# Optimization experiments

Measured on AMD Instinct MI355X. Metric: run time of the kernel, lower is better.

The kernel has to match this reference:

```python
import jax, jax.numpy as jnp
import numpy as np


def sinusoidal_pe(d, length, dtype=jnp.float32):
    """Standard transformer sin/cos positional encoding along the W axis.
    Returns (d, length): pe[2i, p] = sin(p/10000^(2i/d)), pe[2i+1, p] = cos(...)."""
    pos = jnp.arange(length, dtype=dtype)[None, :]            # (1, W)
    i = jnp.arange(0, d, 2, dtype=dtype)[:, None]             # (d//2, 1)
    div = jnp.exp(-i * (np.log(10000.0) / d))                 # (d//2, 1)
    ang = pos * div                                           # (d//2, W)
    pe = jnp.zeros((d, length), dtype)
    pe = pe.at[0::2].set(jnp.sin(ang)).at[1::2].set(jnp.cos(ang))
    return pe


def setup_inputs() -> dict:
    key = jax.random.key(0)
    ks = jax.random.split(key, 8)
    B, C, D, H, W = 2, 64, 32, 64, 96
    q_k_dim = 32
    s = 1.0 / np.sqrt(C)
    return {
        "x": jax.random.normal(ks[0], (B, C, D, H, W), jnp.float32),
        "Wq": jax.random.normal(ks[1], (q_k_dim, C), jnp.float32) * s,
        "bq": jax.random.normal(ks[2], (q_k_dim,), jnp.float32) * 0.01,
        "Wk": jax.random.normal(ks[3], (q_k_dim, C), jnp.float32) * s,
        "bk": jax.random.normal(ks[4], (q_k_dim,), jnp.float32) * 0.01,
        "Wv": jax.random.normal(ks[5], (C, C), jnp.float32) * s,
        "bv": jax.random.normal(ks[6], (C,), jnp.float32) * 0.01,
        "gamma": jax.random.normal(ks[7], (1,), jnp.float32) * 0.1,
    }


def reference(x, Wq, bq, Wk, bk, Wv, bv, gamma):
    # x: (B, C, D, H, W)
    B, C, D, H, W = x.shape
    qk = Wq.shape[0]
    # 1x1x1 Conv3d == per-voxel channel matmul
    Q = jnp.einsum('bcdhw,qc->bqdhw', x, Wq) + bq[None, :, None, None, None]
    K = jnp.einsum('bcdhw,qc->bqdhw', x, Wk) + bk[None, :, None, None, None]
    V = jnp.einsum('bcdhw,vc->bvdhw', x, Wv) + bv[None, :, None, None, None]
    # additive sinusoidal positional encoding along the row (W) axis
    pe_qk = sinusoidal_pe(qk, W, x.dtype)[None, :, None, None, :]
    pe_v = sinusoidal_pe(C, W, x.dtype)[None, :, None, None, :]
    Q = Q + pe_qk
    K = K + pe_qk
    V = V + pe_v
    # row attention: scores over the W axis, independently per (b, d, h)
    # attn[b,d,h,i,j] = sum_q Q[b,q,d,h,i] * K[b,q,d,h,j]  (no 1/sqrt(d) scaling, as in source)
    attn = jax.nn.softmax(jnp.einsum('bqdhi,bqdhj->bdhij', Q, K), axis=-1)
    # out[b,c,d,h,i] = sum_j V[b,c,d,h,j] * attn[b,d,h,i,j]
    out = jnp.einsum('bcdhj,bdhij->bcdhi', V, attn)
    return gamma * out + x
```

## Files before the change

### kernel.cpp

```cpp
#include <hip/hip_runtime.h>
#include <hip/hip_bf16.h>
#include <math.h>

constexpr int Cc = 64, Dd = 32, Hh = 64, Ww = 96, QKd = 32;
constexpr int CSTRIDE = Dd * Hh * Ww;
constexpr int BDIM = 256;

#define FREQ_QK 0.28782313662425574f
#define FREQ_V  0.14391156831212787f
#define LOG2E   1.44269504088896340736f

typedef __bf16 bf16_t;
typedef bf16_t bf16x8 __attribute__((ext_vector_type(8)));
typedef bf16_t bf16x4 __attribute__((ext_vector_type(4)));
typedef float  floatx4 __attribute__((ext_vector_type(4)));

constexpr int XS_STRIDE = 72;
constexpr int QS_STRIDE = 32;
constexpr int VS_STRIDE = 104;
constexpr int PS_STRIDE = 104;
constexpr int OFF_QS = 6912;
constexpr int OFF_KS = 6912 + 3072;
constexpr int OFF_VS = OFF_KS + 3072;
constexpr int SMEM_ELEMS = OFF_VS + 6656;

__global__ __launch_bounds__(BDIM, 4)
void row_attn_mfma(const float* __restrict__ x,
                   const float* __restrict__ Wq, const float* __restrict__ bq,
                   const float* __restrict__ Wk, const float* __restrict__ bk,
                   const float* __restrict__ Wv, const float* __restrict__ bv,
                   const float* __restrict__ gamma,
                   float* __restrict__ y)
{
    __shared__ __align__(16) bf16_t smem[SMEM_ELEMS];
    bf16_t* Xs = smem;
    bf16_t* Ps = smem;
    bf16_t* Qs = smem + OFF_QS;
    bf16_t* Ks = smem + OFF_KS;
    bf16_t* Vs = smem + OFF_VS;

    const int t    = threadIdx.x;
    const int lane = t & 63;
    const int wid  = t >> 6;
    const int l16  = lane & 15;
    const int quad = lane >> 4;

    const int bid = blockIdx.x;
    const int b   = bid / (Dd * Hh);
    const int rem = bid % (Dd * Hh);
    const int d   = rem / Hh;
    const int h   = rem % Hh;
    const int base0 = b * (Cc * CSTRIDE) + d * (Hh * Ww) + h * Ww;

#pragma unroll
    for (int k = 0; k < 12; ++k) {
        int idx = t + k * BDIM;
        int w  = idx % Ww;
        int c  = (idx / Ww) * 2;
        float v0 = x[base0 + c * CSTRIDE + w];
        float v1 = x[base0 + (c + 1) * CSTRIDE + w];
        unsigned short u0 = __builtin_bit_cast(unsigned short, (bf16_t)v0);
        unsigned short u1 = __builtin_bit_cast(unsigned short, (bf16_t)v1);
        *(unsigned int*)(&Xs[w * XS_STRIDE + c]) = (unsigned)u0 | ((unsigned)u1 << 16);
    }

    const float* Wmat = (wid == 0) ? Wq : (wid == 1) ? Wk : Wv;
    const float* bias = (wid == 0) ? bq : (wid == 1) ? bk : bv;
    const float freqc = (wid < 2) ? FREQ_QK : FREQ_V;
    const int   mbase = (wid == 3) ? 32 : 0;

    bf16x8 wfrag[2][2];
#pragma unroll
    for (int mt = 0; mt < 2; ++mt)
#pragma unroll
        for (int kt = 0; kt < 2; ++kt) {
            const float* p = Wmat + (mbase + mt * 16 + l16) * 64 + kt * 32 + quad * 8;
            float4 lo = *(const float4*)p;
            float4 hi = *(const float4*)(p + 4);
            bf16x8 f;
            f[0] = (bf16_t)lo.x; f[1] = (bf16_t)lo.y; f[2] = (bf16_t)lo.z; f[3] = (bf16_t)lo.w;
            f[4] = (bf16_t)hi.x; f[5] = (bf16_t)hi.y; f[6] = (bf16_t)hi.z; f[7] = (bf16_t)hi.w;
            wfrag[mt][kt] = f;
        }
    float biasv[2][4], freq2[2][2];
#pragma unroll
    for (int mt = 0; mt < 2; ++mt) {
#pragma unroll
        for (int r = 0; r < 4; ++r)
            biasv[mt][r] = bias[mbase + mt * 16 + quad * 4 + r];
#pragma unroll
        for (int p2 = 0; p2 < 2; ++p2)
            freq2[mt][p2] = __expf(-(float)(mbase + mt * 16 + quad * 4 + 2 * p2) * freqc);
    }
    __syncthreads();

    bf16_t* dstQK = (wid == 0) ? Qs : Ks;
#pragma unroll
    for (int nt = 0; nt < 6; ++nt) {
        bf16x8 bfr[2];
#pragma unroll
        for (int kt = 0; kt < 2; ++kt)
            bfr[kt] = *(const bf16x8*)(&Xs[(nt * 16 + l16) * XS_STRIDE + kt * 32 + quad * 8]);
#pragma unroll
        for (int mt = 0; mt < 2; ++mt) {
            floatx4 acc = {0.f, 0.f, 0.f, 0.f};
            acc = __builtin_amdgcn_mfma_f32_16x16x32_bf16(wfrag[mt][0], bfr[0], acc, 0, 0, 0);
            acc = __builtin_amdgcn_mfma_f32_16x16x32_bf16(wfrag[mt][1], bfr[1], acc, 0, 0, 0);
            float wv = (float)(nt * 16 + l16);
            float out[4];
#pragma unroll
            for (int p2 = 0; p2 < 2; ++p2) {
                float sn, cs;
                __sincosf(wv * freq2[mt][p2], &sn, &cs);
                out[2 * p2]     = acc[2 * p2]     + biasv[mt][2 * p2]     + sn;
                out[2 * p2 + 1] = acc[2 * p2 + 1] + biasv[mt][2 * p2 + 1] + cs;
            }
            if (wid < 2) {
                if (wid == 0) {
#pragma unroll
                    for (int r = 0; r < 4; ++r) out[r] *= LOG2E;
                }
                bf16x4 pk;
                pk[0] = (bf16_t)out[0]; pk[1] = (bf16_t)out[1];
                pk[2] = (bf16_t)out[2]; pk[3] = (bf16_t)out[3];
                const int w  = nt * 16 + l16;
                const int el = (w * QS_STRIDE + mt * 16 + quad * 4) ^ ((w & 7) << 3);
                *(bf16x4*)(&dstQK[el]) = pk;
            } else {
#pragma unroll
                for (int r = 0; r < 4; ++r)
                    Vs[(mbase + mt * 16 + quad * 4 + r) * VS_STRIDE + nt * 16 + l16] = (bf16_t)out[r];
            }
        }
    }
    __syncthreads();

    const int it0 = (wid < 2) ? wid * 2 : wid + 2;
    const int itc = (wid < 2) ? 2 : 1;
    bf16x8 qfr[2];
#pragma unroll
    for (int ii = 0; ii < 2; ++ii) {
        const int it = it0 + ((itc == 2) ? ii : 0);
        const int w  = it * 16 + l16;
        qfr[ii] = *(const bf16x8*)(&Qs[(w * QS_STRIDE + quad * 8) ^ ((w & 7) << 3)]);
    }
    bf16x8 kfr[6];
#pragma unroll
    for (int jt = 0; jt < 6; ++jt) {
        const int w = jt * 16 + l16;
        kfr[jt] = *(const bf16x8*)(&Ks[(w * QS_STRIDE + quad * 8) ^ ((w & 7) << 3)]);
    }
    __syncthreads();

    for (int ii = 0; ii < itc; ++ii) {
        const int it = it0 + ii;
        floatx4 sacc[6];
#pragma unroll
        for (int jt = 0; jt < 6; ++jt) {
            floatx4 z = {0.f, 0.f, 0.f, 0.f};
            sacc[jt] = __builtin_amdgcn_mfma_f32_16x16x32_bf16(kfr[jt], qfr[ii], z, 0, 0, 0);
        }
        float mr[6];
#pragma unroll
        for (int jt = 0; jt < 6; ++jt)
            mr[jt] = fmaxf(fmaxf(sacc[jt][0], sacc[jt][1]), fmaxf(sacc[jt][2], sacc[jt][3]));
        float m = fmaxf(fmaxf(fmaxf(mr[0], mr[1]), fmaxf(mr[2], mr[3])), fmaxf(mr[4], mr[5]));
        m = fmaxf(m, __shfl_xor(m, 16));
        m = fmaxf(m, __shfl_xor(m, 32));
        float sum = 0.f;
#pragma unroll
        for (int jt = 0; jt < 6; ++jt) {
#pragma unroll
            for (int r = 0; r < 4; ++r) {
                float e = exp2f(sacc[jt][r] - m);
                sacc[jt][r] = e;
                sum += e;
            }
        }
        sum += __shfl_xor(sum, 16);
        sum += __shfl_xor(sum, 32);
        const float inv = __builtin_amdgcn_rcpf(sum);
        const int row = it * 16 + l16;
#pragma unroll
        for (int jt = 0; jt < 6; ++jt) {
            bf16x4 pk;
            pk[0] = (bf16_t)(sacc[jt][0] * inv);
            pk[1] = (bf16_t)(sacc[jt][1] * inv);
            pk[2] = (bf16_t)(sacc[jt][2] * inv);
            pk[3] = (bf16_t)(sacc[jt][3] * inv);
            *(bf16x4*)(&Ps[row * PS_STRIDE + jt * 16 + quad * 4]) = pk;
        }
    }
    __syncthreads();

    const float g = gamma[0];
    const int ct = wid;
    bf16x8 vfr[3];
#pragma unroll
    for (int ks = 0; ks < 3; ++ks)
        vfr[ks] = *(const bf16x8*)(&Vs[(ct * 16 + l16) * VS_STRIDE + ks * 32 + quad * 8]);
#pragma unroll
    for (int it = 0; it < 6; ++it) {
        floatx4 acc = {0.f, 0.f, 0.f, 0.f};
#pragma unroll
        for (int ks = 0; ks < 3; ++ks) {
            bf16x8 bfr = *(const bf16x8*)(&Ps[(it * 16 + l16) * PS_STRIDE + ks * 32 + quad * 8]);
            acc = __builtin_amdgcn_mfma_f32_16x16x32_bf16(vfr[ks], bfr, acc, 0, 0, 0);
        }
#pragma unroll
        for (int r = 0; r < 4; ++r) {
            int c  = ct * 16 + quad * 4 + r;
            int gi = base0 + c * CSTRIDE + it * 16 + l16;
            y[gi] = fmaf(g, acc[r], x[gi]);
        }
    }
}

extern "C" void kernel_launch(void* const* d_in, const int* in_sizes, int n_in,
                              void* d_out, int out_size, void* d_ws, size_t ws_size,
                              hipStream_t stream) {
    const float* x     = (const float*)d_in[0];
    const float* Wq    = (const float*)d_in[1];
    const float* bq    = (const float*)d_in[2];
    const float* Wk    = (const float*)d_in[3];
    const float* bk    = (const float*)d_in[4];
    const float* Wv    = (const float*)d_in[5];
    const float* bv    = (const float*)d_in[6];
    const float* gamma = (const float*)d_in[7];
    float* y = (float*)d_out;

    dim3 grid(2 * 32 * 64);
    row_attn_mfma<<<grid, BDIM, 0, stream>>>(x, Wq, bq, Wk, bk, Wv, bv, gamma, y);
}
```

Before: 214.2 us.

## Process four rows per block with register prefetch of next row

Each block now handles four consecutive H rows, loading the next row's x values into registers while the current row is computed. Weight fragments, biases and positional-encoding seeds are set up once per block. Per-column sincos is replaced by an angle-addition rotation recurrence. This trades fewer, longer-lived blocks and higher register pressure for amortized setup and overlapped global loads.

```diff
diff --git a/kernel.cpp b/kernel.cpp
--- a/kernel.cpp
+++ b/kernel.cpp
@@ -5,6 +5,7 @@
 constexpr int Cc = 64, Dd = 32, Hh = 64, Ww = 96, QKd = 32;
 constexpr int CSTRIDE = Dd * Hh * Ww;
 constexpr int BDIM = 256;
+constexpr int ROWS = 4;
 
 #define FREQ_QK 0.28782313662425574f
 #define FREQ_V  0.14391156831212787f
@@ -20,9 +21,9 @@
 constexpr int VS_STRIDE = 104;
 constexpr int PS_STRIDE = 104;
 constexpr int OFF_QS = 6912;
-constexpr int OFF_KS = 6912 + 3072;
-constexpr int OFF_VS = OFF_KS + 3072;
-constexpr int SMEM_ELEMS = OFF_VS + 6656;
+constexpr int OFF_KS = 9984;
+constexpr int OFF_VS = 13056;
+constexpr int SMEM_ELEMS = 19712;
 
 __global__ __launch_bounds__(BDIM, 4)
 void row_attn_mfma(const float* __restrict__ x,
@@ -45,23 +46,22 @@
     const int l16  = lane & 15;
     const int quad = lane >> 4;
 
-    const int bid = blockIdx.x;
-    const int b   = bid / (Dd * Hh);
-    const int rem = bid % (Dd * Hh);
-    const int d   = rem / Hh;
-    const int h   = rem % Hh;
-    const int base0 = b * (Cc * CSTRIDE) + d * (Hh * Ww) + h * Ww;
-
+    const int row0 = blockIdx.x * ROWS;
+    const int b    = row0 / (Dd * Hh);
+    const int rem  = row0 % (Dd * Hh);
+    const int d    = rem / Hh;
+    const int h    = rem % Hh;
+    int base_row = b * (Cc * CSTRIDE) + d * (Hh * Ww) + h * Ww;
+
+    float raw[24];
 #pragma unroll
     for (int k = 0; k < 12; ++k) {
         int idx = t + k * BDIM;
-        int w  = idx % Ww;
-        int c  = (idx / Ww) * 2;
-        float v0 = x[base0 + c * CSTRIDE + w];
-        float v1 = x[base0 + (c + 1) * CSTRIDE + w];
-        unsigned short u0 = __builtin_bit_cast(unsigned short, (bf16_t)v0);
-        unsigned short u1 = __builtin_bit_cast(unsigned short, (bf16_t)v1);
-        *(unsigned int*)(&Xs[w * XS_STRIDE + c]) = (unsigned)u0 | ((unsigned)u1 << 16);
+        int w   = idx % Ww;
+        int c   = (idx / Ww) * 2;
+        const float* p = x + base_row + c * CSTRIDE + w;
+        raw[2 * k]     = p[0];
+        raw[2 * k + 1] = p[CSTRIDE];
     }
 
     const float* Wmat = (wid == 0) ? Wq : (wid == 1) ? Wk : Wv;
@@ -82,137 +82,190 @@
             f[4] = (bf16_t)hi.x; f[5] = (bf16_t)hi.y; f[6] = (bf16_t)hi.z; f[7] = (bf16_t)hi.w;
             wfrag[mt][kt] = f;
         }
-    float biasv[2][4], freq2[2][2];
-#pragma unroll
-    for (int mt = 0; mt < 2; ++mt) {
+    float biasv[2][4];
+#pragma unroll
+    for (int mt = 0; mt < 2; ++mt)
 #pragma unroll
         for (int r = 0; r < 4; ++r)
             biasv[mt][r] = bias[mbase + mt * 16 + quad * 4 + r];
-#pragma unroll
-        for (int p2 = 0; p2 < 2; ++p2)
-            freq2[mt][p2] = __expf(-(float)(mbase + mt * 16 + quad * 4 + 2 * p2) * freqc);
+
+    float As[4], Ac[4], Rs[4], Rc[4];
+#pragma unroll
+    for (int mt = 0; mt < 2; ++mt)
+#pragma unroll
+        for (int p2 = 0; p2 < 2; ++p2) {
+            float f = __expf(-(float)(mbase + mt * 16 + quad * 4 + 2 * p2) * freqc);
+            int p = mt * 2 + p2;
+            __sincosf((float)l16 * f, &As[p], &Ac[p]);
+            __sincosf(16.0f * f,      &Rs[p], &Rc[p]);
+        }
+
+    unsigned xpack[12];
+#pragma unroll
+    for (int k = 0; k < 12; ++k) {
+        unsigned short u0 = __builtin_bit_cast(unsigned short, (bf16_t)raw[2 * k]);
+        unsigned short u1 = __builtin_bit_cast(unsigned short, (bf16_t)raw[2 * k + 1]);
+        xpack[k] = (unsigned)u0 | ((unsigned)u1 << 16);
     }
-    __syncthreads();
-
-    bf16_t* dstQK = (wid == 0) ? Qs : Ks;
-#pragma unroll
-    for (int nt = 0; nt < 6; ++nt) {
-        bf16x8 bfr[2];
-#pragma unroll
-        for (int kt = 0; kt < 2; ++kt)
-            bfr[kt] = *(const bf16x8*)(&Xs[(nt * 16 + l16) * XS_STRIDE + kt * 32 + quad * 8]);
-#pragma unroll
-        for (int mt = 0; mt < 2; ++mt) {
+
+    const float g   = gamma[0];
+    const int   it0 = (wid < 2) ? wid * 2 : wid + 2;
+    const int   itc = (wid < 2) ? 2 : 1;
+    bf16_t* dstQK   = (wid == 0) ? Qs : Ks;
+
+    for (int row = 0; row < ROWS; ++row) {
+        __syncthreads();
+
+#pragma unroll
+        for (int k = 0; k < 12; ++k) {
+            int idx = t + k * BDIM;
+            int w   = idx % Ww;
+            int c   = (idx / Ww) * 2;
+            *(unsigned*)(&smem[w * XS_STRIDE + c]) = xpack[k];
+        }
+
+        if (row + 1 < ROWS) {
+#pragma unroll
+            for (int k = 0; k < 12; ++k) {
+                int idx = t + k * BDIM;
+                int w   = idx % Ww;
+                int c   = (idx / Ww) * 2;
+                const float* p = x + (base_row + Ww) + c * CSTRIDE + w;
+                raw[2 * k]     = p[0];
+                raw[2 * k + 1] = p[CSTRIDE];
+            }
+        }
+        __syncthreads();
+
+        float sn[4], cs[4];
+#pragma unroll
+        for (int p = 0; p < 4; ++p) { sn[p] = As[p]; cs[p] = Ac[p]; }
+#pragma unroll
+        for (int nt = 0; nt < 6; ++nt) {
+            bf16x8 bfr[2];
+#pragma unroll
+            for (int kt = 0; kt < 2; ++kt)
+                bfr[kt] = *(const bf16x8*)(&Xs[(nt * 16 + l16) * XS_STRIDE + kt * 32 + quad * 8]);
+#pragma unroll
+            for (int mt = 0; mt < 2; ++mt) {
+                floatx4 acc = {0.f, 0.f, 0.f, 0.f};
+                acc = __builtin_amdgcn_mfma_f32_16x16x32_bf16(wfrag[mt][0], bfr[0], acc, 0, 0, 0);
+                acc = __builtin_amdgcn_mfma_f32_16x16x32_bf16(wfrag[mt][1], bfr[1], acc, 0, 0, 0);
+                float out[4];
+#pragma unroll
+                for (int p2 = 0; p2 < 2; ++p2) {
+                    int p = mt * 2 + p2;
+                    out[2 * p2]     = acc[2 * p2]     + biasv[mt][2 * p2]     + sn[p];
+                    out[2 * p2 + 1] = acc[2 * p2 + 1] + biasv[mt][2 * p2 + 1] + cs[p];
+                }
+                if (wid < 2) {
+                    if (wid == 0) {
+#pragma unroll
+                        for (int r = 0; r < 4; ++r) out[r] *= LOG2E;
+                    }
+                    bf16x4 pk;
+                    pk[0] = (bf16_t)out[0]; pk[1] = (bf16_t)out[1];
+                    pk[2] = (bf16_t)out[2]; pk[3] = (bf16_t)out[3];
+                    const int w  = nt * 16 + l16;
+                    const int el = (w * QS_STRIDE + mt * 16 + quad * 4) ^ ((w & 7) << 3);
+                    *(bf16x4*)(&dstQK[el]) = pk;
+                } else {
+#pragma unroll
+                    for (int r = 0; r < 4; ++r)
+                        Vs[(mbase + mt * 16 + quad * 4 + r) * VS_STRIDE + nt * 16 + l16] = (bf16_t)out[r];
+                }
+            }
+#pragma unroll
+            for (int p = 0; p < 4; ++p) {
+                float tsn = sn[p] * Rc[p] + cs[p] * Rs[p];
+                cs[p] = cs[p] * Rc[p] - sn[p] * Rs[p];
+                sn[p] = tsn;
+            }
+        }
+
+        if (row + 1 < ROWS) {
+#pragma unroll
+            for (int k = 0; k < 12; ++k) {
+                unsigned short u0 = __builtin_bit_cast(unsigned short, (bf16_t)raw[2 * k]);
+                unsigned short u1 = __builtin_bit_cast(unsigned short, (bf16_t)raw[2 * k + 1]);
+                xpack[k] = (unsigned)u0 | ((unsigned)u1 << 16);
+            }
+        }
+        __syncthreads();
+
+        bf16x8 qfr[2];
+#pragma unroll
+        for (int ii = 0; ii < 2; ++ii) {
+            const int it = it0 + ((itc == 2) ? ii : 0);
+            const int w  = it * 16 + l16;
+            qfr[ii] = *(const bf16x8*)(&Qs[(w * QS_STRIDE + quad * 8) ^ ((w & 7) << 3)]);
+        }
+        __syncthreads();
+
+        for (int ii = 0; ii < itc; ++ii) {
+            const int it = it0 + ii;
+            floatx4 sacc[6];
+#pragma unroll
+            for (int jt = 0; jt < 6; ++jt) {
+                const int w = jt * 16 + l16;
+                bf16x8 afr = *(const bf16x8*)(&Ks[(w * QS_STRIDE + quad * 8) ^ ((w & 7) << 3)]);
+                floatx4 z = {0.f, 0.f, 0.f, 0.f};
+                sacc[jt] = __builtin_amdgcn_mfma_f32_16x16x32_bf16(afr, qfr[ii], z, 0, 0, 0);
+            }
+            float mr[6];
+#pragma unroll
+            for (int jt = 0; jt < 6; ++jt)
+                mr[jt] = fmaxf(fmaxf(sacc[jt][0], sacc[jt][1]), fmaxf(sacc[jt][2], sacc[jt][3]));
+            float m = fmaxf(fmaxf(fmaxf(mr[0], mr[1]), fmaxf(mr[2], mr[3])), fmaxf(mr[4], mr[5]));
+            m = fmaxf(m, __shfl_xor(m, 16));
+            m = fmaxf(m, __shfl_xor(m, 32));
+            float sum = 0.f;
+#pragma unroll
+            for (int jt = 0; jt < 6; ++jt) {
+#pragma unroll
+                for (int r = 0; r < 4; ++r) {
+                    float e = exp2f(sacc[jt][r] - m);
+                    sacc[jt][r] = e;
+                    sum += e;
+                }
+            }
+            sum += __shfl_xor(sum, 16);
+            sum += __shfl_xor(sum, 32);
+            const float inv = __builtin_amdgcn_rcpf(sum);
+            const int row_i = it * 16 + l16;
+#pragma unroll
+            for (int jt = 0; jt < 6; ++jt) {
+                bf16x4 pk;
+                pk[0] = (bf16_t)(sacc[jt][0] * inv);
+                pk[1] = (bf16_t)(sacc[jt][1] * inv);
+                pk[2] = (bf16_t)(sacc[jt][2] * inv);
+                pk[3] = (bf16_t)(sacc[jt][3] * inv);
+                *(bf16x4*)(&Ps[row_i * PS_STRIDE + jt * 16 + quad * 4]) = pk;
+            }
+        }
+        __syncthreads();
+
+        bf16x8 vfr[3];
+#pragma unroll
+        for (int ks = 0; ks < 3; ++ks)
+            vfr[ks] = *(const bf16x8*)(&Vs[(wid * 16 + l16) * VS_STRIDE + ks * 32 + quad * 8]);
+#pragma unroll
+        for (int it = 0; it < 6; ++it) {
             floatx4 acc = {0.f, 0.f, 0.f, 0.f};
-            acc = __builtin_amdgcn_mfma_f32_16x16x32_bf16(wfrag[mt][0], bfr[0], acc, 0, 0, 0);
-            acc = __builtin_amdgcn_mfma_f32_16x16x32_bf16(wfrag[mt][1], bfr[1], acc, 0, 0, 0);
-            float wv = (float)(nt * 16 + l16);
-            float out[4];
-#pragma unroll
-            for (int p2 = 0; p2 < 2; ++p2) {
-                float sn, cs;
-                __sincosf(wv * freq2[mt][p2], &sn, &cs);
-                out[2 * p2]     = acc[2 * p2]     + biasv[mt][2 * p2]     + sn;
-                out[2 * p2 + 1] = acc[2 * p2 + 1] + biasv[mt][2 * p2 + 1] + cs;
-            }
-            if (wid < 2) {
-                if (wid == 0) {
-#pragma unroll
-                    for (int r = 0; r < 4; ++r) out[r] *= LOG2E;
-                }
-                bf16x4 pk;
-                pk[0] = (bf16_t)out[0]; pk[1] = (bf16_t)out[1];
-                pk[2] = (bf16_t)out[2]; pk[3] = (bf16_t)out[3];
-                const int w  = nt * 16 + l16;
-                const int el = (w * QS_STRIDE + mt * 16 + quad * 4) ^ ((w & 7) << 3);
-                *(bf16x4*)(&dstQK[el]) = pk;
-            } else {
-#pragma unroll
-                for (int r = 0; r < 4; ++r)
-                    Vs[(mbase + mt * 16 + quad * 4 + r) * VS_STRIDE + nt * 16 + l16] = (bf16_t)out[r];
-            }
-        }
-    }
-    __syncthreads();
-
-    const int it0 = (wid < 2) ? wid * 2 : wid + 2;
-    const int itc = (wid < 2) ? 2 : 1;
-    bf16x8 qfr[2];
-#pragma unroll
-    for (int ii = 0; ii < 2; ++ii) {
-        const int it = it0 + ((itc == 2) ? ii : 0);
-        const int w  = it * 16 + l16;
-        qfr[ii] = *(const bf16x8*)(&Qs[(w * QS_STRIDE + quad * 8) ^ ((w & 7) << 3)]);
-    }
-    bf16x8 kfr[6];
-#pragma unroll
-    for (int jt = 0; jt < 6; ++jt) {
-        const int w = jt * 16 + l16;
-        kfr[jt] = *(const bf16x8*)(&Ks[(w * QS_STRIDE + quad * 8) ^ ((w & 7) << 3)]);
-    }
-    __syncthreads();
-
-    for (int ii = 0; ii < itc; ++ii) {
-        const int it = it0 + ii;
-        floatx4 sacc[6];
-#pragma unroll
-        for (int jt = 0; jt < 6; ++jt) {
-            floatx4 z = {0.f, 0.f, 0.f, 0.f};
-            sacc[jt] = __builtin_amdgcn_mfma_f32_16x16x32_bf16(kfr[jt], qfr[ii], z, 0, 0, 0);
-        }
-        float mr[6];
-#pragma unroll
-        for (int jt = 0; jt < 6; ++jt)
-            mr[jt] = fmaxf(fmaxf(sacc[jt][0], sacc[jt][1]), fmaxf(sacc[jt][2], sacc[jt][3]));
-        float m = fmaxf(fmaxf(fmaxf(mr[0], mr[1]), fmaxf(mr[2], mr[3])), fmaxf(mr[4], mr[5]));
-        m = fmaxf(m, __shfl_xor(m, 16));
-        m = fmaxf(m, __shfl_xor(m, 32));
-        float sum = 0.f;
-#pragma unroll
-        for (int jt = 0; jt < 6; ++jt) {
+#pragma unroll
+            for (int ks = 0; ks < 3; ++ks) {
+                bf16x8 bfr = *(const bf16x8*)(&Ps[(it * 16 + l16) * PS_STRIDE + ks * 32 + quad * 8]);
+                acc = __builtin_amdgcn_mfma_f32_16x16x32_bf16(vfr[ks], bfr, acc, 0, 0, 0);
+            }
 #pragma unroll
             for (int r = 0; r < 4; ++r) {
-                float e = exp2f(sacc[jt][r] - m);
-                sacc[jt][r] = e;
-                sum += e;
-            }
-        }
-        sum += __shfl_xor(sum, 16);
-        sum += __shfl_xor(sum, 32);
-        const float inv = __builtin_amdgcn_rcpf(sum);
-        const int row = it * 16 + l16;
-#pragma unroll
-        for (int jt = 0; jt < 6; ++jt) {
-            bf16x4 pk;
-            pk[0] = (bf16_t)(sacc[jt][0] * inv);
-            pk[1] = (bf16_t)(sacc[jt][1] * inv);
-            pk[2] = (bf16_t)(sacc[jt][2] * inv);
-            pk[3] = (bf16_t)(sacc[jt][3] * inv);
-            *(bf16x4*)(&Ps[row * PS_STRIDE + jt * 16 + quad * 4]) = pk;
-        }
-    }
-    __syncthreads();
-
-    const float g = gamma[0];
-    const int ct = wid;
-    bf16x8 vfr[3];
-#pragma unroll
-    for (int ks = 0; ks < 3; ++ks)
-        vfr[ks] = *(const bf16x8*)(&Vs[(ct * 16 + l16) * VS_STRIDE + ks * 32 + quad * 8]);
-#pragma unroll
-    for (int it = 0; it < 6; ++it) {
-        floatx4 acc = {0.f, 0.f, 0.f, 0.f};
-#pragma unroll
-        for (int ks = 0; ks < 3; ++ks) {
-            bf16x8 bfr = *(const bf16x8*)(&Ps[(it * 16 + l16) * PS_STRIDE + ks * 32 + quad * 8]);
-            acc = __builtin_amdgcn_mfma_f32_16x16x32_bf16(vfr[ks], bfr, acc, 0, 0, 0);
-        }
-#pragma unroll
-        for (int r = 0; r < 4; ++r) {
-            int c  = ct * 16 + quad * 4 + r;
-            int gi = base0 + c * CSTRIDE + it * 16 + l16;
-            y[gi] = fmaf(g, acc[r], x[gi]);
-        }
+                int c  = wid * 16 + quad * 4 + r;
+                int gi = base_row + c * CSTRIDE + it * 16 + l16;
+                y[gi] = fmaf(g, acc[r], x[gi]);
+            }
+        }
+
+        base_row += Ww;
     }
 }
 
@@ -229,6 +282,6 @@
     const float* gamma = (const float*)d_in[7];
     float* y = (float*)d_out;
 
-    dim3 grid(2 * 32 * 64);
+    dim3 grid((2 * 32 * 64) / ROWS);
     row_attn_mfma<<<grid, BDIM, 0, stream>>>(x, Wq, bq, Wk, bk, Wv, bv, gamma, y);
 }
```

Result: slower. 353.7 us (+65.1%).

## Precompute PE+bias table, drop softmax max, defer normalization to output

Applied to the files above, without the earlier changes.

A small pre-kernel writes a per-position table of sinusoidal encoding plus bias, with the log2e scale folded in for Q. The main kernel then reads that table instead of evaluating sincos and exp per element. Softmax no longer subtracts the row max. Normalization by the row sum is deferred: gamma/sum is kept per row in shared memory and applied in the output FMA. K fragments are now loaded from LDS inside the score loop instead of being held in registers. This cuts transcendental work, shuffle reductions and register pressure, at the cost of an extra launch and a risk of exp2 overflow when scores grow large.

```diff
diff --git a/kernel.cpp b/kernel.cpp
--- a/kernel.cpp
+++ b/kernel.cpp
@@ -20,16 +20,40 @@
 constexpr int VS_STRIDE = 104;
 constexpr int PS_STRIDE = 104;
 constexpr int OFF_QS = 6912;
-constexpr int OFF_KS = 6912 + 3072;
-constexpr int OFF_VS = OFF_KS + 3072;
-constexpr int SMEM_ELEMS = OFF_VS + 6656;
+constexpr int OFF_KS = 9984;
+constexpr int OFF_VS = 13056;
+constexpr int OFF_LS = 19712;
+constexpr int SMEM_ELEMS = 19712 + 192;
+
+__global__ void pe_bias_fill(const float* __restrict__ bq,
+                             const float* __restrict__ bk,
+                             const float* __restrict__ bv,
+                             float* __restrict__ ws)
+{
+    int i = blockIdx.x * blockDim.x + threadIdx.x;
+    if (i < 96 * 32) {
+        int w = i >> 5, q = i & 31;
+        float f = __expf(-(float)(q & ~1) * FREQ_QK);
+        float s, c; __sincosf((float)w * f, &s, &c);
+        float pe = (q & 1) ? c : s;
+        ws[i]        = (pe + bq[q]) * LOG2E;
+        ws[3072 + i] =  pe + bk[q];
+    } else if (i < 96 * 32 + 96 * 64) {
+        int j = i - 96 * 32;
+        int w = j >> 6, c = j & 63;
+        float f = __expf(-(float)(c & ~1) * FREQ_V);
+        float s, cc; __sincosf((float)w * f, &s, &cc);
+        ws[6144 + j] = ((c & 1) ? cc : s) + bv[c];
+    }
+}
 
 __global__ __launch_bounds__(BDIM, 4)
 void row_attn_mfma(const float* __restrict__ x,
-                   const float* __restrict__ Wq, const float* __restrict__ bq,
-                   const float* __restrict__ Wk, const float* __restrict__ bk,
-                   const float* __restrict__ Wv, const float* __restrict__ bv,
+                   const float* __restrict__ Wq,
+                   const float* __restrict__ Wk,
+                   const float* __restrict__ Wv,
                    const float* __restrict__ gamma,
+                   const float* __restrict__ pet,
                    float* __restrict__ y)
 {
     __shared__ __align__(16) bf16_t smem[SMEM_ELEMS];
@@ -38,6 +62,7 @@
     bf16_t* Qs = smem + OFF_QS;
     bf16_t* Ks = smem + OFF_KS;
     bf16_t* Vs = smem + OFF_VS;
+    float*  Lsf = (float*)(smem + OFF_LS);
 
     const int t    = threadIdx.x;
     const int lane = t & 63;
@@ -65,8 +90,6 @@
     }
 
     const float* Wmat = (wid == 0) ? Wq : (wid == 1) ? Wk : Wv;
-    const float* bias = (wid == 0) ? bq : (wid == 1) ? bk : bv;
-    const float freqc = (wid < 2) ? FREQ_QK : FREQ_V;
     const int   mbase = (wid == 3) ? 32 : 0;
 
     bf16x8 wfrag[2][2];
@@ -82,16 +105,12 @@
             f[4] = (bf16_t)hi.x; f[5] = (bf16_t)hi.y; f[6] = (bf16_t)hi.z; f[7] = (bf16_t)hi.w;
             wfrag[mt][kt] = f;
         }
-    float biasv[2][4], freq2[2][2];
-#pragma unroll
-    for (int mt = 0; mt < 2; ++mt) {
-#pragma unroll
-        for (int r = 0; r < 4; ++r)
-            biasv[mt][r] = bias[mbase + mt * 16 + quad * 4 + r];
-#pragma unroll
-        for (int p2 = 0; p2 < 2; ++p2)
-            freq2[mt][p2] = __expf(-(float)(mbase + mt * 16 + quad * 4 + 2 * p2) * freqc);
-    }
+
+    const float* tbl  = (wid == 0) ? pet : (wid == 1) ? pet + 3072 : pet + 6144;
+    const int    tstr = (wid < 2) ? 32 : 64;
+    const float  ascl = (wid == 0) ? LOG2E : 1.0f;
+    const float  g    = gamma[0];
+
     __syncthreads();
 
     bf16_t* dstQK = (wid == 0) ? Qs : Ks;
@@ -106,20 +125,13 @@
             floatx4 acc = {0.f, 0.f, 0.f, 0.f};
             acc = __builtin_amdgcn_mfma_f32_16x16x32_bf16(wfrag[mt][0], bfr[0], acc, 0, 0, 0);
             acc = __builtin_amdgcn_mfma_f32_16x16x32_bf16(wfrag[mt][1], bfr[1], acc, 0, 0, 0);
-            float wv = (float)(nt * 16 + l16);
+            const float4 pe4 = *(const float4*)(&tbl[(nt * 16 + l16) * tstr + mbase + mt * 16 + quad * 4]);
             float out[4];
-#pragma unroll
-            for (int p2 = 0; p2 < 2; ++p2) {
-                float sn, cs;
-                __sincosf(wv * freq2[mt][p2], &sn, &cs);
-                out[2 * p2]     = acc[2 * p2]     + biasv[mt][2 * p2]     + sn;
-                out[2 * p2 + 1] = acc[2 * p2 + 1] + biasv[mt][2 * p2 + 1] + cs;
-            }
+            out[0] = fmaf(acc[0], ascl, pe4.x);
+            out[1] = fmaf(acc[1], ascl, pe4.y);
+            out[2] = fmaf(acc[2], ascl, pe4.z);
+            out[3] = fmaf(acc[3], ascl, pe4.w);
             if (wid < 2) {
-                if (wid == 0) {
-#pragma unroll
-                    for (int r = 0; r < 4; ++r) out[r] *= LOG2E;
-                }
                 bf16x4 pk;
                 pk[0] = (bf16_t)out[0]; pk[1] = (bf16_t)out[1];
                 pk[2] = (bf16_t)out[2]; pk[3] = (bf16_t)out[3];
@@ -144,12 +156,6 @@
         const int w  = it * 16 + l16;
         qfr[ii] = *(const bf16x8*)(&Qs[(w * QS_STRIDE + quad * 8) ^ ((w & 7) << 3)]);
     }
-    bf16x8 kfr[6];
-#pragma unroll
-    for (int jt = 0; jt < 6; ++jt) {
-        const int w = jt * 16 + l16;
-        kfr[jt] = *(const bf16x8*)(&Ks[(w * QS_STRIDE + quad * 8) ^ ((w & 7) << 3)]);
-    }
     __syncthreads();
 
     for (int ii = 0; ii < itc; ++ii) {
@@ -157,48 +163,36 @@
         floatx4 sacc[6];
 #pragma unroll
         for (int jt = 0; jt < 6; ++jt) {
+            const int w = jt * 16 + l16;
+            bf16x8 afr = *(const bf16x8*)(&Ks[(w * QS_STRIDE + quad * 8) ^ ((w & 7) << 3)]);
             floatx4 z = {0.f, 0.f, 0.f, 0.f};
-            sacc[jt] = __builtin_amdgcn_mfma_f32_16x16x32_bf16(kfr[jt], qfr[ii], z, 0, 0, 0);
-        }
-        float mr[6];
-#pragma unroll
-        for (int jt = 0; jt < 6; ++jt)
-            mr[jt] = fmaxf(fmaxf(sacc[jt][0], sacc[jt][1]), fmaxf(sacc[jt][2], sacc[jt][3]));
-        float m = fmaxf(fmaxf(fmaxf(mr[0], mr[1]), fmaxf(mr[2], mr[3])), fmaxf(mr[4], mr[5]));
-        m = fmaxf(m, __shfl_xor(m, 16));
-        m = fmaxf(m, __shfl_xor(m, 32));
+            sacc[jt] = __builtin_amdgcn_mfma_f32_16x16x32_bf16(afr, qfr[ii], z, 0, 0, 0);
+        }
+        const int row_i = it * 16 + l16;
         float sum = 0.f;
 #pragma unroll
         for (int jt = 0; jt < 6; ++jt) {
-#pragma unroll
-            for (int r = 0; r < 4; ++r) {
-                float e = exp2f(sacc[jt][r] - m);
-                sacc[jt][r] = e;
-                sum += e;
-            }
+            float e0 = exp2f(sacc[jt][0]);
+            float e1 = exp2f(sacc[jt][1]);
+            float e2 = exp2f(sacc[jt][2]);
+            float e3 = exp2f(sacc[jt][3]);
+            sum += (e0 + e1) + (e2 + e3);
+            bf16x4 pk;
+            pk[0] = (bf16_t)e0; pk[1] = (bf16_t)e1;
+            pk[2] = (bf16_t)e2; pk[3] = (bf16_t)e3;
+            *(bf16x4*)(&Ps[row_i * PS_STRIDE + jt * 16 + quad * 4]) = pk;
         }
         sum += __shfl_xor(sum, 16);
         sum += __shfl_xor(sum, 32);
-        const float inv = __builtin_amdgcn_rcpf(sum);
-        const int row = it * 16 + l16;
-#pragma unroll
-        for (int jt = 0; jt < 6; ++jt) {
-            bf16x4 pk;
-            pk[0] = (bf16_t)(sacc[jt][0] * inv);
-            pk[1] = (bf16_t)(sacc[jt][1] * inv);
-            pk[2] = (bf16_t)(sacc[jt][2] * inv);
-            pk[3] = (bf16_t)(sacc[jt][3] * inv);
-            *(bf16x4*)(&Ps[row * PS_STRIDE + jt * 16 + quad * 4]) = pk;
-        }
-    }
-    __syncthreads();
-
-    const float g = gamma[0];
-    const int ct = wid;
+        if (quad == 0)
+            Lsf[row_i] = g * __builtin_amdgcn_rcpf(sum);
+    }
+    __syncthreads();
+
     bf16x8 vfr[3];
 #pragma unroll
     for (int ks = 0; ks < 3; ++ks)
-        vfr[ks] = *(const bf16x8*)(&Vs[(ct * 16 + l16) * VS_STRIDE + ks * 32 + quad * 8]);
+        vfr[ks] = *(const bf16x8*)(&Vs[(wid * 16 + l16) * VS_STRIDE + ks * 32 + quad * 8]);
 #pragma unroll
     for (int it = 0; it < 6; ++it) {
         floatx4 acc = {0.f, 0.f, 0.f, 0.f};
@@ -207,11 +201,12 @@
             bf16x8 bfr = *(const bf16x8*)(&Ps[(it * 16 + l16) * PS_STRIDE + ks * 32 + quad * 8]);
             acc = __builtin_amdgcn_mfma_f32_16x16x32_bf16(vfr[ks], bfr, acc, 0, 0, 0);
         }
+        const float invg = Lsf[it * 16 + l16];
 #pragma unroll
         for (int r = 0; r < 4; ++r) {
-            int c  = ct * 16 + quad * 4 + r;
+            int c  = wid * 16 + quad * 4 + r;
             int gi = base0 + c * CSTRIDE + it * 16 + l16;
-            y[gi] = fmaf(g, acc[r], x[gi]);
+            y[gi] = fmaf(acc[r], invg, x[gi]);
         }
     }
 }
@@ -227,8 +222,11 @@
     const float* Wv    = (const float*)d_in[5];
     const float* bv    = (const float*)d_in[6];
     const float* gamma = (const float*)d_in[7];
-    float* y = (float*)d_out;
+    float* y  = (float*)d_out;
+    float* ws = (float*)d_ws;
+
+    pe_bias_fill<<<36, 256, 0, stream>>>(bq, bk, bv, ws);
 
     dim3 grid(2 * 32 * 64);
-    row_attn_mfma<<<grid, BDIM, 0, stream>>>(x, Wq, bq, Wk, bk, Wv, bv, gamma, y);
+    row_attn_mfma<<<grid, BDIM, 0, stream>>>(x, Wq, Wk, Wv, gamma, ws, y);
 }
```

After: 232.0 us. 1.08x slower.

## Split row-attention block across eight waves and defer softmax normalization

Applied to the files above, without the earlier changes.

Doubles the block to 512 threads so eight waves each take half of the projection, score and output tiles. The fp32 x values are loaded into registers before the weight fetch, to overlap global latency. The softmax max-subtraction is dropped, and normalization is deferred: gamma times the reciprocal of the row sum goes into a small LDS array and is applied in the output epilogue. This trades more waves per CU and fewer ALU ops for a risk of exp2 overflow when scores are large.

```diff
diff --git a/kernel.cpp b/kernel.cpp
--- a/kernel.cpp
+++ b/kernel.cpp
@@ -4,7 +4,7 @@
 
 constexpr int Cc = 64, Dd = 32, Hh = 64, Ww = 96, QKd = 32;
 constexpr int CSTRIDE = Dd * Hh * Ww;
-constexpr int BDIM = 256;
+constexpr int BDIM = 512;
 
 #define FREQ_QK 0.28782313662425574f
 #define FREQ_V  0.14391156831212787f
@@ -20,11 +20,12 @@
 constexpr int VS_STRIDE = 104;
 constexpr int PS_STRIDE = 104;
 constexpr int OFF_QS = 6912;
-constexpr int OFF_KS = 6912 + 3072;
-constexpr int OFF_VS = OFF_KS + 3072;
-constexpr int SMEM_ELEMS = OFF_VS + 6656;
-
-__global__ __launch_bounds__(BDIM, 4)
+constexpr int OFF_KS = 9984;
+constexpr int OFF_VS = 13056;
+constexpr int OFF_LS = 19712;
+constexpr int SMEM_ELEMS = 19712 + 192;
+
+__global__ __launch_bounds__(BDIM, 8)
 void row_attn_mfma(const float* __restrict__ x,
                    const float* __restrict__ Wq, const float* __restrict__ bq,
                    const float* __restrict__ Wk, const float* __restrict__ bk,
@@ -38,10 +39,11 @@
     bf16_t* Qs = smem + OFF_QS;
     bf16_t* Ks = smem + OFF_KS;
     bf16_t* Vs = smem + OFF_VS;
+    float*  Lsf = (float*)(smem + OFF_LS);
 
     const int t    = threadIdx.x;
+    const int wid  = t >> 6;
     const int lane = t & 63;
-    const int wid  = t >> 6;
     const int l16  = lane & 15;
     const int quad = lane >> 4;
 
@@ -52,22 +54,23 @@
     const int h   = rem % Hh;
     const int base0 = b * (Cc * CSTRIDE) + d * (Hh * Ww) + h * Ww;
 
-#pragma unroll
-    for (int k = 0; k < 12; ++k) {
+    float raw[12];
+#pragma unroll
+    for (int k = 0; k < 6; ++k) {
         int idx = t + k * BDIM;
-        int w  = idx % Ww;
-        int c  = (idx / Ww) * 2;
-        float v0 = x[base0 + c * CSTRIDE + w];
-        float v1 = x[base0 + (c + 1) * CSTRIDE + w];
-        unsigned short u0 = __builtin_bit_cast(unsigned short, (bf16_t)v0);
-        unsigned short u1 = __builtin_bit_cast(unsigned short, (bf16_t)v1);
-        *(unsigned int*)(&Xs[w * XS_STRIDE + c]) = (unsigned)u0 | ((unsigned)u1 << 16);
-    }
-
-    const float* Wmat = (wid == 0) ? Wq : (wid == 1) ? Wk : Wv;
-    const float* bias = (wid == 0) ? bq : (wid == 1) ? bk : bv;
-    const float freqc = (wid < 2) ? FREQ_QK : FREQ_V;
-    const int   mbase = (wid == 3) ? 32 : 0;
+        int w   = idx % Ww;
+        int c   = (idx / Ww) * 2;
+        const float* p = x + base0 + c * CSTRIDE + w;
+        raw[2 * k]     = p[0];
+        raw[2 * k + 1] = p[CSTRIDE];
+    }
+
+    const float* Wmat  = (wid < 2) ? Wq : (wid < 4) ? Wk : Wv;
+    const float* bias  = (wid < 2) ? bq : (wid < 4) ? bk : bv;
+    const float  freqc = (wid < 4) ? FREQ_QK : FREQ_V;
+    const int    mbase = (wid >= 6) ? 32 : 0;
+    const int    nt0   = (wid & 1) * 3;
+    const float  g     = gamma[0];
 
     bf16x8 wfrag[2][2];
 #pragma unroll
@@ -82,7 +85,7 @@
             f[4] = (bf16_t)hi.x; f[5] = (bf16_t)hi.y; f[6] = (bf16_t)hi.z; f[7] = (bf16_t)hi.w;
             wfrag[mt][kt] = f;
         }
-    float biasv[2][4], freq2[2][2];
+    float biasv[2][4], fr[4];
 #pragma unroll
     for (int mt = 0; mt < 2; ++mt) {
 #pragma unroll
@@ -90,33 +93,44 @@
             biasv[mt][r] = bias[mbase + mt * 16 + quad * 4 + r];
 #pragma unroll
         for (int p2 = 0; p2 < 2; ++p2)
-            freq2[mt][p2] = __expf(-(float)(mbase + mt * 16 + quad * 4 + 2 * p2) * freqc);
-    }
-    __syncthreads();
-
-    bf16_t* dstQK = (wid == 0) ? Qs : Ks;
-#pragma unroll
-    for (int nt = 0; nt < 6; ++nt) {
+            fr[mt * 2 + p2] = __expf(-(float)(mbase + mt * 16 + quad * 4 + 2 * p2) * freqc);
+    }
+
+#pragma unroll
+    for (int k = 0; k < 6; ++k) {
+        int idx = t + k * BDIM;
+        int w   = idx % Ww;
+        int c   = (idx / Ww) * 2;
+        unsigned short u0 = __builtin_bit_cast(unsigned short, (bf16_t)raw[2 * k]);
+        unsigned short u1 = __builtin_bit_cast(unsigned short, (bf16_t)raw[2 * k + 1]);
+        *(unsigned*)(&smem[w * XS_STRIDE + c]) = (unsigned)u0 | ((unsigned)u1 << 16);
+    }
+    __syncthreads();
+
+    bf16_t* dstQK = (wid < 2) ? Qs : Ks;
+#pragma unroll
+    for (int ni = 0; ni < 3; ++ni) {
+        const int nt = nt0 + ni;
         bf16x8 bfr[2];
 #pragma unroll
         for (int kt = 0; kt < 2; ++kt)
             bfr[kt] = *(const bf16x8*)(&Xs[(nt * 16 + l16) * XS_STRIDE + kt * 32 + quad * 8]);
+        const float wv = (float)(nt * 16 + l16);
 #pragma unroll
         for (int mt = 0; mt < 2; ++mt) {
             floatx4 acc = {0.f, 0.f, 0.f, 0.f};
             acc = __builtin_amdgcn_mfma_f32_16x16x32_bf16(wfrag[mt][0], bfr[0], acc, 0, 0, 0);
             acc = __builtin_amdgcn_mfma_f32_16x16x32_bf16(wfrag[mt][1], bfr[1], acc, 0, 0, 0);
-            float wv = (float)(nt * 16 + l16);
             float out[4];
 #pragma unroll
             for (int p2 = 0; p2 < 2; ++p2) {
                 float sn, cs;
-                __sincosf(wv * freq2[mt][p2], &sn, &cs);
+                __sincosf(wv * fr[mt * 2 + p2], &sn, &cs);
                 out[2 * p2]     = acc[2 * p2]     + biasv[mt][2 * p2]     + sn;
                 out[2 * p2 + 1] = acc[2 * p2 + 1] + biasv[mt][2 * p2 + 1] + cs;
             }
-            if (wid < 2) {
-                if (wid == 0) {
+            if (wid < 4) {
+                if (wid < 2) {
 #pragma unroll
                     for (int r = 0; r < 4; ++r) out[r] *= LOG2E;
                 }
@@ -135,83 +149,64 @@
     }
     __syncthreads();
 
-    const int it0 = (wid < 2) ? wid * 2 : wid + 2;
-    const int itc = (wid < 2) ? 2 : 1;
-    bf16x8 qfr[2];
-#pragma unroll
-    for (int ii = 0; ii < 2; ++ii) {
-        const int it = it0 + ((itc == 2) ? ii : 0);
-        const int w  = it * 16 + l16;
-        qfr[ii] = *(const bf16x8*)(&Qs[(w * QS_STRIDE + quad * 8) ^ ((w & 7) << 3)]);
-    }
-    bf16x8 kfr[6];
-#pragma unroll
-    for (int jt = 0; jt < 6; ++jt) {
-        const int w = jt * 16 + l16;
-        kfr[jt] = *(const bf16x8*)(&Ks[(w * QS_STRIDE + quad * 8) ^ ((w & 7) << 3)]);
-    }
-    __syncthreads();
-
-    for (int ii = 0; ii < itc; ++ii) {
-        const int it = it0 + ii;
+    bf16x8 qfr;
+    if (wid < 6) {
+        const int w = wid * 16 + l16;
+        qfr = *(const bf16x8*)(&Qs[(w * QS_STRIDE + quad * 8) ^ ((w & 7) << 3)]);
+    }
+    __syncthreads();
+
+    if (wid < 6) {
         floatx4 sacc[6];
 #pragma unroll
         for (int jt = 0; jt < 6; ++jt) {
+            const int w = jt * 16 + l16;
+            bf16x8 afr = *(const bf16x8*)(&Ks[(w * QS_STRIDE + quad * 8) ^ ((w & 7) << 3)]);
             floatx4 z = {0.f, 0.f, 0.f, 0.f};
-            sacc[jt] = __builtin_amdgcn_mfma_f32_16x16x32_bf16(kfr[jt], qfr[ii], z, 0, 0, 0);
-        }
-        float mr[6];
-#pragma unroll
-        for (int jt = 0; jt < 6; ++jt)
-            mr[jt] = fmaxf(fmaxf(sacc[jt][0], sacc[jt][1]), fmaxf(sacc[jt][2], sacc[jt][3]));
-        float m = fmaxf(fmaxf(fmaxf(mr[0], mr[1]), fmaxf(mr[2], mr[3])), fmaxf(mr[4], mr[5]));
-        m = fmaxf(m, __shfl_xor(m, 16));
-        m = fmaxf(m, __shfl_xor(m, 32));
+            sacc[jt] = __builtin_amdgcn_mfma_f32_16x16x32_bf16(afr, qfr, z, 0, 0, 0);
+        }
+        const int row_i = wid * 16 + l16;
         float sum = 0.f;
 #pragma unroll
         for (int jt = 0; jt < 6; ++jt) {
-#pragma unroll
-            for (int r = 0; r < 4; ++r) {
-                float e = exp2f(sacc[jt][r] - m);
-                sacc[jt][r] = e;
-                sum += e;
-            }
+            float e0 = exp2f(sacc[jt][0]);
+            float e1 = exp2f(sacc[jt][1]);
+            float e2 = exp2f(sacc[jt][2]);
+            float e3 = exp2f(sacc[jt][3]);
+            sum += (e0 + e1) + (e2 + e3);
+            bf16x4 pk;
+            pk[0] = (bf16_t)e0; pk[1] = (bf16_t)e1;
+            pk[2] = (bf16_t)e2; pk[3] = (bf16_t)e3;
+            *(bf16x4*)(&Ps[row_i * PS_STRIDE + jt * 16 + quad * 4]) = pk;
         }
         sum += __shfl_xor(sum, 16);
         sum += __shfl_xor(sum, 32);
-        const float inv = __builtin_amdgcn_rcpf(sum);
-        const int row = it * 16 + l16;
-#pragma unroll
-        for (int jt = 0; jt < 6; ++jt) {
-            bf16x4 pk;
-            pk[0] = (bf16_t)(sacc[jt][0] * inv);
-            pk[1] = (bf16_t)(sacc[jt][1] * inv);
-            pk[2] = (bf16_t)(sacc[jt][2] * inv);
-            pk[3] = (bf16_t)(sacc[jt][3] * inv);
-            *(bf16x4*)(&Ps[row * PS_STRIDE + jt * 16 + quad * 4]) = pk;
-        }
-    }
-    __syncthreads();
-
-    const float g = gamma[0];
-    const int ct = wid;
+        if (quad == 0)
+            Lsf[row_i] = g * __builtin_amdgcn_rcpf(sum);
+    }
+    __syncthreads();
+
+    const int ct  = wid >> 1;
+    const int itb = (wid & 1) * 3;
     bf16x8 vfr[3];
 #pragma unroll
     for (int ks = 0; ks < 3; ++ks)
         vfr[ks] = *(const bf16x8*)(&Vs[(ct * 16 + l16) * VS_STRIDE + ks * 32 + quad * 8]);
 #pragma unroll
-    for (int it = 0; it < 6; ++it) {
+    for (int ii = 0; ii < 3; ++ii) {
+        const int itt = itb + ii;
         floatx4 acc = {0.f, 0.f, 0.f, 0.f};
 #pragma unroll
         for (int ks = 0; ks < 3; ++ks) {
-            bf16x8 bfr = *(const bf16x8*)(&Ps[(it * 16 + l16) * PS_STRIDE + ks * 32 + quad * 8]);
+            bf16x8 bfr = *(const bf16x8*)(&Ps[(itt * 16 + l16) * PS_STRIDE + ks * 32 + quad * 8]);
             acc = __builtin_amdgcn_mfma_f32_16x16x32_bf16(vfr[ks], bfr, acc, 0, 0, 0);
         }
+        const float invg = Lsf[itt * 16 + l16];
 #pragma unroll
         for (int r = 0; r < 4; ++r) {
             int c  = ct * 16 + quad * 4 + r;
-            int gi = base0 + c * CSTRIDE + it * 16 + l16;
-            y[gi] = fmaf(g, acc[r], x[gi]);
+            int gi = base0 + c * CSTRIDE + itt * 16 + l16;
+            y[gi] = fmaf(acc[r], invg, x[gi]);
         }
     }
 }
```

Result: slower. 232.8 us (+8.7%).
